# Optimization experiments

Hardware: AMD Instinct MI355X
Metric: run time of the kernel (lower is better)

The kernel has to match this reference:

```python
import jax, jax.numpy as jnp
import numpy as np

D_MODEL = 1024
NHEAD = 16
DK = D_MODEL // NHEAD  # 64
B, S = 2, 2048


def setup_inputs() -> dict:
    key = jax.random.key(0)
    ks = jax.random.split(key, 8)
    Q = jax.random.normal(ks[0], (B, S, D_MODEL), dtype=jnp.float32)
    K = jax.random.normal(ks[1], (B, S, D_MODEL), dtype=jnp.float32)
    V = jax.random.normal(ks[2], (B, S, D_MODEL), dtype=jnp.float32)
    additive_mask = jax.random.normal(ks[3], (S, S), dtype=jnp.float32)
    key_padding_mask = jnp.zeros((B, S), dtype=jnp.int32)  # ignored by the module
    # Per-head projection weights, stacked over heads: [H, d_model, dk]
    scale = 1.0 / np.sqrt(D_MODEL)
    WQ = jax.random.normal(ks[4], (NHEAD, D_MODEL, DK), dtype=jnp.float32) * scale
    WK = jax.random.normal(ks[5], (NHEAD, D_MODEL, DK), dtype=jnp.float32) * scale
    WV = jax.random.normal(ks[6], (NHEAD, D_MODEL, DK), dtype=jnp.float32) * scale
    WO = jax.random.normal(ks[7], (D_MODEL, D_MODEL), dtype=jnp.float32) * scale
    return {"Q": Q, "K": K, "V": V, "additive_mask": additive_mask,
            "key_padding_mask": key_padding_mask,
            "WQ": WQ, "WK": WK, "WV": WV, "WO": WO}


def reference(Q, K, V, additive_mask, key_padding_mask, WQ, WK, WV, WO):
    # Per-head projections, batched over heads: [B, H, S, dk]
    q = jnp.einsum('bsd,hdk->bhsk', Q, WQ)
    k = jnp.einsum('bsd,hdk->bhsk', K, WK)
    v = jnp.einsum('bsd,hdk->bhsk', V, WV)
    # scores: [B, H, S, S]; mask broadcasts over batch and head
    scores = jnp.einsum('bhqk,bhsk->bhqs', q, k) / np.sqrt(DK)
    scores = scores + additive_mask[None, None, :, :]
    attn = jax.nn.softmax(scores, axis=-1)
    o = jnp.einsum('bhqs,bhsk->bhqk', attn, v)  # [B, H, S, dk]
    # concat heads in head order == transpose + reshape to [B, S, H*dk]
    o = o.transpose(0, 2, 1, 3).reshape(Q.shape[0], Q.shape[1], D_MODEL)
    return o @ WO
```

## Files before the change

kernel.cpp:

```cpp
#include <hip/hip_runtime.h>
#include <hip/hip_bf16.h>
#include <stdint.h>

#define D_MODEL 1024
#define NHEAD 16
#define DKH 64
#define BATCH 2
#define SEQ 2048
#define LOG2E 1.44269504088896f

typedef __bf16 bf16_t;
typedef __bf16 bf16x8 __attribute__((ext_vector_type(8)));
typedef float f32x4 __attribute__((ext_vector_type(4)));

__device__ __forceinline__ float fast_exp2(float x) {
#if __has_builtin(__builtin_amdgcn_exp2f)
  return __builtin_amdgcn_exp2f(x);
#else
  return exp2f(x);
#endif
}

__device__ __forceinline__ void gload_lds16(const bf16_t* g, bf16_t* l) {
  auto gp = (const __attribute__((address_space(1))) void*)(uintptr_t)g;
  auto lp = (__attribute__((address_space(3))) void*)(uintptr_t)l;
  __builtin_amdgcn_global_load_lds(gp, lp, 16, 0, 0);
}

__global__ void k_cvtw(const float* __restrict__ WQ, const float* __restrict__ WK,
                       const float* __restrict__ WV, const float* __restrict__ WO,
                       bf16_t* __restrict__ wt) {
  int j = blockIdx.x * 256 + threadIdx.x;
  if (j < 3072 * 1024) {
    int bn = j >> 17, kt = (j >> 12) & 31, u = (j >> 10) & 3;
    int row = (j >> 3) & 127, e = j & 7;
    int n = bn * 128 + row;
    int d = kt * 32 + u * 8 + e;
    int proj = n >> 10, h = (n >> 6) & 15, k = n & 63;
    const float* w = proj == 0 ? WQ : (proj == 1 ? WK : WV);
    float scale = proj == 0 ? (0.125f * LOG2E) : 1.0f;
    wt[j] = (bf16_t)(w[(h << 16) + (d << 6) + k] * scale);
  } else {
    int j2 = j - 3072 * 1024;
    int bn = j2 >> 17, kt = (j2 >> 12) & 31, u = (j2 >> 10) & 3;
    int row = (j2 >> 3) & 127, e = j2 & 7;
    int n = bn * 128 + row;
    int d = kt * 32 + u * 8 + e;
    wt[j] = (bf16_t)WO[(d << 10) + n];
  }
}

__global__ void k_maskg(const float* __restrict__ M, bf16_t* __restrict__ Mf) {
  int t = blockIdx.x * 256 + threadIdx.x;
  int c = t & 3, lane = (t >> 2) & 63;
  int kvt = (t >> 8) & 31, qt16 = t >> 13;
  int q = qt16 * 16 + (lane & 15);
  int kv = kvt * 64 + c * 16 + ((lane >> 4) << 2);
  float4 m4 = *reinterpret_cast<const float4*>(M + (size_t)q * SEQ + kv);
  bf16_t o[4];
  o[0] = (bf16_t)(m4.x * LOG2E); o[1] = (bf16_t)(m4.y * LOG2E);
  o[2] = (bf16_t)(m4.z * LOG2E); o[3] = (bf16_t)(m4.w * LOG2E);
  *reinterpret_cast<ushort4*>(Mf + (size_t)t * 4) = *reinterpret_cast<ushort4*>(o);
}

__device__ __forceinline__ int vperm(int u) {
  return ((u >> 5) << 5) | (((u >> 2) & 3) << 3) | (((u >> 4) & 1) << 2) | (u & 3);
}

__global__ __launch_bounds__(256)
void k_gemm_qkv(const float* __restrict__ Qs, const float* __restrict__ Ks32,
                const float* __restrict__ Vs32, const bf16_t* __restrict__ Bt,
                bf16_t* __restrict__ qh, bf16_t* __restrict__ Kf,
                bf16_t* __restrict__ Vf) {
  __shared__ __align__(16) bf16_t As[4 * 128 * 8];
  __shared__ __align__(16) bf16_t Bs[4 * 128 * 8];
  const int tid = threadIdx.x;
  const int lane = tid & 63, wave = tid >> 6;
  const int g = lane >> 4, lr = lane & 15;
  const int bid = blockIdx.x;
  const int xcd = bid & 7, jj = bid >> 3;
  const int bm = xcd * 4 + (jj & 3);
  const int bn = jj >> 2;
  const int pn = bn >> 3;
  const float* Ap32 = pn == 0 ? Qs : (pn == 1 ? Ks32 : Vs32);
  const bf16_t* btile = Bt + (size_t)bn * 32 * 4096;
  const int wm = (wave >> 1) << 6, wn = (wave & 1) << 6;
  const int arow = tid >> 1, au0 = (tid & 1) << 1, ako = (tid & 1) << 4;
  const float* aptr = Ap32 + (size_t)(bm * 128 + arow) * 1024 + ako;
  f32x4 acc[4][4] = {};

  float4 fA0 = *reinterpret_cast<const float4*>(aptr);
  float4 fA1 = *reinterpret_cast<const float4*>(aptr + 4);
  float4 fA2 = *reinterpret_cast<const float4*>(aptr + 8);
  float4 fA3 = *reinterpret_cast<const float4*>(aptr + 12);

  for (int kt = 0; kt < 1024; kt += 32) {
    const int ktt = kt >> 5;
#pragma unroll
    for (int cc = 0; cc < 2; cc++) {
      int c = tid + cc * 256;
      gload_lds16(btile + (size_t)ktt * 4096 + c * 8, Bs + c * 8);
    }
    {
      bf16x8 o0, o1;
      o0[0] = (bf16_t)fA0.x; o0[1] = (bf16_t)fA0.y; o0[2] = (bf16_t)fA0.z; o0[3] = (bf16_t)fA0.w;
      o0[4] = (bf16_t)fA1.x; o0[5] = (bf16_t)fA1.y; o0[6] = (bf16_t)fA1.z; o0[7] = (bf16_t)fA1.w;
      o1[0] = (bf16_t)fA2.x; o1[1] = (bf16_t)fA2.y; o1[2] = (bf16_t)fA2.z; o1[3] = (bf16_t)fA2.w;
      o1[4] = (bf16_t)fA3.x; o1[5] = (bf16_t)fA3.y; o1[6] = (bf16_t)fA3.z; o1[7] = (bf16_t)fA3.w;
      *reinterpret_cast<bf16x8*>(As + (au0 * 128 + arow) * 8) = o0;
      *reinterpret_cast<bf16x8*>(As + ((au0 + 1) * 128 + arow) * 8) = o1;
    }
    if (kt + 32 < 1024) {
      const float* np = aptr + kt + 32;
      fA0 = *reinterpret_cast<const float4*>(np);
      fA1 = *reinterpret_cast<const float4*>(np + 4);
      fA2 = *reinterpret_cast<const float4*>(np + 8);
      fA3 = *reinterpret_cast<const float4*>(np + 12);
    }
    __syncthreads();
    bf16x8 af[4], bfr[4];
#pragma unroll
    for (int t = 0; t < 4; t++)
      af[t] = *reinterpret_cast<const bf16x8*>(As + (g * 128 + wm + t * 16 + lr) * 8);
#pragma unroll
    for (int t = 0; t < 4; t++)
      bfr[t] = *reinterpret_cast<const bf16x8*>(Bs + (g * 128 + wn + t * 16 + lr) * 8);
    __builtin_amdgcn_s_setprio(1);
#pragma unroll
    for (int i = 0; i < 4; i++)
#pragma unroll
      for (int j = 0; j < 4; j++)
        acc[i][j] = __builtin_amdgcn_mfma_f32_16x16x32_bf16(af[i], bfr[j], acc[i][j], 0, 0, 0);
    __builtin_amdgcn_s_setprio(0);
    __syncthreads();
  }

#pragma unroll
  for (int i = 0; i < 4; i++)
#pragma unroll
    for (int j = 0; j < 4; j++)
#pragma unroll
      for (int e = 0; e < 4; e++) {
        int row = (bm << 7) + wm + i * 16 + g * 4 + e;
        int col = ((bn & 7) << 7) + wn + j * 16 + lr;
        float v = acc[i][j][e];
        int b = row >> 11, s = row & 2047, h = col >> 6, d = col & 63;
        size_t tilebase = ((size_t)(((b << 4) + h) * 32) + (s >> 6)) * 4096;
        if (pn == 0) {
          qh[((size_t)(((b << 4) + h) * SEQ + s) << 6) + d] = (bf16_t)v;
        } else if (pn == 1) {
          int r = s & 63, u = (d >> 3) ^ (r & 7), e2 = d & 7;
          Kf[tilebase + r * 64 + u * 8 + e2] = (bf16_t)v;
        } else {
          int c6 = vperm(s & 63);
          int u = (c6 >> 3) ^ (d & 7), e2 = c6 & 7;
          Vf[tilebase + d * 64 + u * 8 + e2] = (bf16_t)v;
        }
      }
}

__global__ __launch_bounds__(256)
void k_gemm_wo(const bf16_t* __restrict__ A, const bf16_t* __restrict__ Bt,
               float* __restrict__ C) {
  __shared__ __align__(16) bf16_t As[64 * 32];
  __shared__ __align__(16) bf16_t Bs[4 * 128 * 8];
  const int tid = threadIdx.x;
  const int lane = tid & 63, wave = tid >> 6;
  const int g = lane >> 4, lr = lane & 15;
  const int bid = blockIdx.x;
  const int xcd = bid & 7, jj = bid >> 3;
  const int bm = xcd * 8 + (jj & 7);
  const int bn = jj >> 3;
  const bf16_t* btile = Bt + (size_t)bn * 32 * 4096;
  const int wm = (wave >> 1) << 5, wn = (wave & 1) << 6;
  f32x4 acc[2][4] = {};

  for (int kt = 0; kt < 1024; kt += 32) {
    const int ktt = kt >> 5;
    {
      int row = tid >> 2, ko = (tid & 3) << 3;
      gload_lds16(A + (size_t)(bm * 64 + row) * 1024 + kt + ko, As + tid * 8);
    }
#pragma unroll
    for (int cc = 0; cc < 2; cc++) {
      int c = tid + cc * 256;
      gload_lds16(btile + (size_t)ktt * 4096 + c * 8, Bs + c * 8);
    }
    __syncthreads();
    bf16x8 af[2], bfr[4];
#pragma unroll
    for (int t = 0; t < 2; t++)
      af[t] = *reinterpret_cast<const bf16x8*>(As + (wm + t * 16 + lr) * 32 + g * 8);
#pragma unroll
    for (int t = 0; t < 4; t++)
      bfr[t] = *reinterpret_cast<const bf16x8*>(Bs + (g * 128 + wn + t * 16 + lr) * 8);
    __builtin_amdgcn_s_setprio(1);
#pragma unroll
    for (int i = 0; i < 2; i++)
#pragma unroll
      for (int j = 0; j < 4; j++)
        acc[i][j] = __builtin_amdgcn_mfma_f32_16x16x32_bf16(af[i], bfr[j], acc[i][j], 0, 0, 0);
    __builtin_amdgcn_s_setprio(0);
    __syncthreads();
  }
#pragma unroll
  for (int i = 0; i < 2; i++)
#pragma unroll
    for (int j = 0; j < 4; j++)
#pragma unroll
      for (int e = 0; e < 4; e++) {
        int row = (bm << 6) + wm + i * 16 + g * 4 + e;
        int col = (bn << 7) + wn + j * 16 + lr;
        C[(size_t)row * D_MODEL + col] = acc[i][j][e];
      }
}

__global__ __launch_bounds__(512)
void k_attn4(const bf16_t* __restrict__ Qh, const bf16_t* __restrict__ Kf,
             const bf16_t* __restrict__ Vf, const bf16_t* __restrict__ Mf,
             bf16_t* __restrict__ O) {
  __shared__ __align__(16) bf16_t Ks[2][64 * 64];
  __shared__ __align__(16) bf16_t Vs[2][64 * 64];
  const int bid = blockIdx.x;
  const int xcd = bid & 7, loc = bid >> 3;
  const int bh = xcd * 4 + (loc >> 4);
  const int qtile = loc & 15;
  const int b = bh >> 4, h = bh & 15;
  const int tid = threadIdx.x, wave = tid >> 6, lane = tid & 63;
  const int g = lane >> 4, lr = lane & 15;
  const int qbase = qtile * 128 + wave * 16;
  const bf16_t* qp = Qh + (size_t)bh * SEQ * DKH;
  const bf16_t* kfp = Kf + (size_t)bh * 32 * 4096;
  const bf16_t* vfp = Vf + (size_t)bh * 32 * 4096;
  const int qt16 = qtile * 8 + wave;
  const bf16_t* mp = Mf + ((size_t)qt16 * 32 * 64 + lane) * 16;

  bf16x8 aq[2];
#pragma unroll
  for (int ks = 0; ks < 2; ks++)
    aq[ks] = *reinterpret_cast<const bf16x8*>(
        qp + (size_t)(qbase + lr) * DKH + ks * 32 + g * 8);

  f32x4 oacc[4] = {};
  f32x4 lacc = {};
  const bf16_t onev = (bf16_t)1.0f;
  const bf16x8 ones = {onev, onev, onev, onev, onev, onev, onev, onev};

  auto stage = [&](int buf, int kt) {
    gload_lds16(kfp + (size_t)kt * 4096 + tid * 8, &Ks[buf][tid * 8]);
    gload_lds16(vfp + (size_t)kt * 4096 + tid * 8, &Vs[buf][tid * 8]);
  };

  stage(0, 0);
  bf16x8 mva = *reinterpret_cast<const bf16x8*>(mp);
  bf16x8 mvb = *reinterpret_cast<const bf16x8*>(mp + 8);
  __syncthreads();

  for (int it = 0; it < SEQ / 64; ++it) {
    const int cur = it & 1;
    if (it + 1 < SEQ / 64) stage(cur ^ 1, it + 1);
    bf16x8 mna = mva, mnb = mvb;
    if (it + 1 < SEQ / 64) {
      const bf16_t* mn = mp + (size_t)(it + 1) * 1024;
      mna = *reinterpret_cast<const bf16x8*>(mn);
      mnb = *reinterpret_cast<const bf16x8*>(mn + 8);
    }

    const bf16_t* kb = Ks[cur];
    const bf16_t* vb = Vs[cur];

    f32x4 p[4];
#pragma unroll
    for (int c = 0; c < 4; c++) {
      int r = c * 16 + lr;
      bf16x8 bk0 = *reinterpret_cast<const bf16x8*>(kb + r * 64 + ((g ^ (lr & 7)) << 3));
      bf16x8 bk1 = *reinterpret_cast<const bf16x8*>(kb + r * 64 + (((4 + g) ^ (lr & 7)) << 3));
      __builtin_amdgcn_s_setprio(1);
      f32x4 a = {};
      a = __builtin_amdgcn_mfma_f32_16x16x32_bf16(bk0, aq[0], a, 0, 0, 0);
      a = __builtin_amdgcn_mfma_f32_16x16x32_bf16(bk1, aq[1], a, 0, 0, 0);
      __builtin_amdgcn_s_setprio(0);
      p[c] = a;
    }

    bf16x8 pa[2];
#pragma unroll
    for (int c = 0; c < 4; c++)
#pragma unroll
      for (int e = 0; e < 4; e++) {
        int idx = c * 4 + e;
        float mk = (float)(idx < 8 ? mva[idx] : mvb[idx - 8]);
        float x = p[c][e] + mk;
        float pe = fast_exp2(fminf(x, 60.f));
        pa[c >> 1][(c & 1) * 4 + e] = (bf16_t)pe;
      }

    lacc = __builtin_amdgcn_mfma_f32_16x16x32_bf16(pa[0], ones, lacc, 0, 0, 0);
    lacc = __builtin_amdgcn_mfma_f32_16x16x32_bf16(pa[1], ones, lacc, 0, 0, 0);

#pragma unroll
    for (int c2 = 0; c2 < 4; c2++) {
      int r = c2 * 16 + lr;
      bf16x8 bv0 = *reinterpret_cast<const bf16x8*>(vb + r * 64 + ((g ^ (lr & 7)) << 3));
      bf16x8 bv1 = *reinterpret_cast<const bf16x8*>(vb + r * 64 + (((4 + g) ^ (lr & 7)) << 3));
      __builtin_amdgcn_s_setprio(1);
      oacc[c2] = __builtin_amdgcn_mfma_f32_16x16x32_bf16(pa[0], bv0, oacc[c2], 0, 0, 0);
      oacc[c2] = __builtin_amdgcn_mfma_f32_16x16x32_bf16(pa[1], bv1, oacc[c2], 0, 0, 0);
      __builtin_amdgcn_s_setprio(0);
    }
    __syncthreads();
    mva = mna; mvb = mnb;
  }

  float inv[4];
#pragma unroll
  for (int e = 0; e < 4; e++) inv[e] = 1.0f / lacc[e];
#pragma unroll
  for (int c2 = 0; c2 < 4; c2++)
#pragma unroll
    for (int e = 0; e < 4; e++) {
      float v = oacc[c2][e] * inv[e];
      int row = qbase + g * 4 + e;
      int col = (h << 6) + c2 * 16 + lr;
      O[(size_t)(b * SEQ + row) * D_MODEL + col] = (bf16_t)v;
    }
}

extern "C" void kernel_launch(void* const* d_in, const int* in_sizes, int n_in,
                              void* d_out, int out_size, void* d_ws, size_t ws_size,
                              hipStream_t stream) {
  const float* Q  = (const float*)d_in[0];
  const float* K  = (const float*)d_in[1];
  const float* V  = (const float*)d_in[2];
  const float* M  = (const float*)d_in[3];
  const float* WQ = (const float*)d_in[5];
  const float* WK = (const float*)d_in[6];
  const float* WV = (const float*)d_in[7];
  const float* WO = (const float*)d_in[8];

  char* ws = (char*)d_ws;
  const size_t MB = 1 << 20;
  bf16_t* Mf    = (bf16_t*)(ws + 24 * MB);
  bf16_t* WqkvT = (bf16_t*)(ws + 32 * MB);
  bf16_t* WoT   = (bf16_t*)(ws + 38 * MB);
  bf16_t* qh    = (bf16_t*)(ws + 40 * MB);
  bf16_t* Kf    = (bf16_t*)(ws + 48 * MB);
  bf16_t* Vf    = (bf16_t*)(ws + 56 * MB);
  bf16_t* Ob    = (bf16_t*)(ws + 64 * MB);

  k_maskg<<<4096, 256, 0, stream>>>(M, Mf);
  k_cvtw<<<16384, 256, 0, stream>>>(WQ, WK, WV, WO, WqkvT);

  k_gemm_qkv<<<768, 256, 0, stream>>>(Q, K, V, WqkvT, qh, Kf, Vf);

  k_attn4<<<512, 512, 0, stream>>>(qh, Kf, Vf, Mf, Ob);

  k_gemm_wo<<<512, 256, 0, stream>>>(Ob, WoT, (float*)d_out);
}
```

Before: 135.7 us.

## Double-buffer LDS tiles in QKV and output projection GEMMs

Both projection GEMM kernels switch from single-buffered LDS to ping-pong buffers, so the next K-tile is loaded (and the fp32 A tile converted) into the alternate buffer while MFMAs consume the current one. The QKV kernel also keeps two register stages of fp32 A data to prefetch two tiles ahead, and its loop is fully unrolled. This aims to hide global/LDS load latency behind compute and drop one barrier per iteration, at the cost of doubled LDS use and higher register pressure, which may lower occupancy.

Result: slower. 138.5 us (+2.0%).

```diff
diff --git a/kernel.cpp b/kernel.cpp
--- a/kernel.cpp
+++ b/kernel.cpp
@@ -72,8 +72,8 @@
                 const float* __restrict__ Vs32, const bf16_t* __restrict__ Bt,
                 bf16_t* __restrict__ qh, bf16_t* __restrict__ Kf,
                 bf16_t* __restrict__ Vf) {
-  __shared__ __align__(16) bf16_t As[4 * 128 * 8];
-  __shared__ __align__(16) bf16_t Bs[4 * 128 * 8];
+  __shared__ __align__(16) bf16_t As[2][4 * 128 * 8];
+  __shared__ __align__(16) bf16_t Bs[2][4 * 128 * 8];
   const int tid = threadIdx.x;
   const int lane = tid & 63, wave = tid >> 6;
   const int g = lane >> 4, lr = lane & 15;
@@ -89,42 +89,68 @@
   const float* aptr = Ap32 + (size_t)(bm * 128 + arow) * 1024 + ako;
   f32x4 acc[4][4] = {};
 
-  float4 fA0 = *reinterpret_cast<const float4*>(aptr);
-  float4 fA1 = *reinterpret_cast<const float4*>(aptr + 4);
-  float4 fA2 = *reinterpret_cast<const float4*>(aptr + 8);
-  float4 fA3 = *reinterpret_cast<const float4*>(aptr + 12);
-
-  for (int kt = 0; kt < 1024; kt += 32) {
-    const int ktt = kt >> 5;
-#pragma unroll
-    for (int cc = 0; cc < 2; cc++) {
-      int c = tid + cc * 256;
-      gload_lds16(btile + (size_t)ktt * 4096 + c * 8, Bs + c * 8);
-    }
-    {
+  float4 sA[4], sB[4];
+#pragma unroll
+  for (int i = 0; i < 4; i++) sA[i] = *reinterpret_cast<const float4*>(aptr + i * 4);
+  {
+    bf16x8 o0, o1;
+    o0[0] = (bf16_t)sA[0].x; o0[1] = (bf16_t)sA[0].y; o0[2] = (bf16_t)sA[0].z; o0[3] = (bf16_t)sA[0].w;
+    o0[4] = (bf16_t)sA[1].x; o0[5] = (bf16_t)sA[1].y; o0[6] = (bf16_t)sA[1].z; o0[7] = (bf16_t)sA[1].w;
+    o1[0] = (bf16_t)sA[2].x; o1[1] = (bf16_t)sA[2].y; o1[2] = (bf16_t)sA[2].z; o1[3] = (bf16_t)sA[2].w;
+    o1[4] = (bf16_t)sA[3].x; o1[5] = (bf16_t)sA[3].y; o1[6] = (bf16_t)sA[3].z; o1[7] = (bf16_t)sA[3].w;
+    *reinterpret_cast<bf16x8*>(&As[0][(au0 * 128 + arow) * 8]) = o0;
+    *reinterpret_cast<bf16x8*>(&As[0][((au0 + 1) * 128 + arow) * 8]) = o1;
+  }
+#pragma unroll
+  for (int cc = 0; cc < 2; cc++) {
+    int c = tid + cc * 256;
+    gload_lds16(btile + c * 8, &Bs[0][c * 8]);
+  }
+#pragma unroll
+  for (int i = 0; i < 4; i++) sB[i] = *reinterpret_cast<const float4*>(aptr + 32 + i * 4);
+  __syncthreads();
+
+#pragma unroll
+  for (int t = 0; t < 32; ++t) {
+    const int c = t & 1;
+    if (t + 1 < 32) {
+#pragma unroll
+      for (int cc = 0; cc < 2; cc++) {
+        int ch = tid + cc * 256;
+        gload_lds16(btile + (size_t)(t + 1) * 4096 + ch * 8, &Bs[c ^ 1][ch * 8]);
+      }
       bf16x8 o0, o1;
-      o0[0] = (bf16_t)fA0.x; o0[1] = (bf16_t)fA0.y; o0[2] = (bf16_t)fA0.z; o0[3] = (bf16_t)fA0.w;
-      o0[4] = (bf16_t)fA1.x; o0[5] = (bf16_t)fA1.y; o0[6] = (bf16_t)fA1.z; o0[7] = (bf16_t)fA1.w;
-      o1[0] = (bf16_t)fA2.x; o1[1] = (bf16_t)fA2.y; o1[2] = (bf16_t)fA2.z; o1[3] = (bf16_t)fA2.w;
-      o1[4] = (bf16_t)fA3.x; o1[5] = (bf16_t)fA3.y; o1[6] = (bf16_t)fA3.z; o1[7] = (bf16_t)fA3.w;
-      *reinterpret_cast<bf16x8*>(As + (au0 * 128 + arow) * 8) = o0;
-      *reinterpret_cast<bf16x8*>(As + ((au0 + 1) * 128 + arow) * 8) = o1;
-    }
-    if (kt + 32 < 1024) {
-      const float* np = aptr + kt + 32;
-      fA0 = *reinterpret_cast<const float4*>(np);
-      fA1 = *reinterpret_cast<const float4*>(np + 4);
-      fA2 = *reinterpret_cast<const float4*>(np + 8);
-      fA3 = *reinterpret_cast<const float4*>(np + 12);
-    }
-    __syncthreads();
+      if ((t & 1) == 0) {
+        o0[0] = (bf16_t)sB[0].x; o0[1] = (bf16_t)sB[0].y; o0[2] = (bf16_t)sB[0].z; o0[3] = (bf16_t)sB[0].w;
+        o0[4] = (bf16_t)sB[1].x; o0[5] = (bf16_t)sB[1].y; o0[6] = (bf16_t)sB[1].z; o0[7] = (bf16_t)sB[1].w;
+        o1[0] = (bf16_t)sB[2].x; o1[1] = (bf16_t)sB[2].y; o1[2] = (bf16_t)sB[2].z; o1[3] = (bf16_t)sB[2].w;
+        o1[4] = (bf16_t)sB[3].x; o1[5] = (bf16_t)sB[3].y; o1[6] = (bf16_t)sB[3].z; o1[7] = (bf16_t)sB[3].w;
+      } else {
+        o0[0] = (bf16_t)sA[0].x; o0[1] = (bf16_t)sA[0].y; o0[2] = (bf16_t)sA[0].z; o0[3] = (bf16_t)sA[0].w;
+        o0[4] = (bf16_t)sA[1].x; o0[5] = (bf16_t)sA[1].y; o0[6] = (bf16_t)sA[1].z; o0[7] = (bf16_t)sA[1].w;
+        o1[0] = (bf16_t)sA[2].x; o1[1] = (bf16_t)sA[2].y; o1[2] = (bf16_t)sA[2].z; o1[3] = (bf16_t)sA[2].w;
+        o1[4] = (bf16_t)sA[3].x; o1[5] = (bf16_t)sA[3].y; o1[6] = (bf16_t)sA[3].z; o1[7] = (bf16_t)sA[3].w;
+      }
+      *reinterpret_cast<bf16x8*>(&As[c ^ 1][(au0 * 128 + arow) * 8]) = o0;
+      *reinterpret_cast<bf16x8*>(&As[c ^ 1][((au0 + 1) * 128 + arow) * 8]) = o1;
+    }
+    if (t + 2 < 32) {
+      const float* np = aptr + (size_t)(t + 2) * 32;
+      if ((t & 1) == 0) {
+#pragma unroll
+        for (int i = 0; i < 4; i++) sA[i] = *reinterpret_cast<const float4*>(np + i * 4);
+      } else {
+#pragma unroll
+        for (int i = 0; i < 4; i++) sB[i] = *reinterpret_cast<const float4*>(np + i * 4);
+      }
+    }
     bf16x8 af[4], bfr[4];
 #pragma unroll
-    for (int t = 0; t < 4; t++)
-      af[t] = *reinterpret_cast<const bf16x8*>(As + (g * 128 + wm + t * 16 + lr) * 8);
-#pragma unroll
-    for (int t = 0; t < 4; t++)
-      bfr[t] = *reinterpret_cast<const bf16x8*>(Bs + (g * 128 + wn + t * 16 + lr) * 8);
+    for (int q = 0; q < 4; q++)
+      af[q] = *reinterpret_cast<const bf16x8*>(&As[c][(g * 128 + wm + q * 16 + lr) * 8]);
+#pragma unroll
+    for (int q = 0; q < 4; q++)
+      bfr[q] = *reinterpret_cast<const bf16x8*>(&Bs[c][(g * 128 + wn + q * 16 + lr) * 8]);
     __builtin_amdgcn_s_setprio(1);
 #pragma unroll
     for (int i = 0; i < 4; i++)
@@ -162,8 +188,8 @@
 __global__ __launch_bounds__(256)
 void k_gemm_wo(const bf16_t* __restrict__ A, const bf16_t* __restrict__ Bt,
                float* __restrict__ C) {
-  __shared__ __align__(16) bf16_t As[64 * 32];
-  __shared__ __align__(16) bf16_t Bs[4 * 128 * 8];
+  __shared__ __align__(16) bf16_t As[2][64 * 32];
+  __shared__ __align__(16) bf16_t Bs[2][4 * 128 * 8];
   const int tid = threadIdx.x;
   const int lane = tid & 63, wave = tid >> 6;
   const int g = lane >> 4, lr = lane & 15;
@@ -175,25 +201,29 @@
   const int wm = (wave >> 1) << 5, wn = (wave & 1) << 6;
   f32x4 acc[2][4] = {};
 
-  for (int kt = 0; kt < 1024; kt += 32) {
-    const int ktt = kt >> 5;
-    {
-      int row = tid >> 2, ko = (tid & 3) << 3;
-      gload_lds16(A + (size_t)(bm * 64 + row) * 1024 + kt + ko, As + tid * 8);
-    }
+  auto stage = [&](int buf, int t) {
+    int row = tid >> 2, ko = (tid & 3) << 3;
+    gload_lds16(A + (size_t)(bm * 64 + row) * 1024 + t * 32 + ko, &As[buf][tid * 8]);
 #pragma unroll
     for (int cc = 0; cc < 2; cc++) {
       int c = tid + cc * 256;
-      gload_lds16(btile + (size_t)ktt * 4096 + c * 8, Bs + c * 8);
-    }
-    __syncthreads();
+      gload_lds16(btile + (size_t)t * 4096 + c * 8, &Bs[buf][c * 8]);
+    }
+  };
+
+  stage(0, 0);
+  __syncthreads();
+
+  for (int t = 0; t < 32; ++t) {
+    const int c = t & 1;
+    if (t + 1 < 32) stage(c ^ 1, t + 1);
     bf16x8 af[2], bfr[4];
 #pragma unroll
-    for (int t = 0; t < 2; t++)
-      af[t] = *reinterpret_cast<const bf16x8*>(As + (wm + t * 16 + lr) * 32 + g * 8);
-#pragma unroll
-    for (int t = 0; t < 4; t++)
-      bfr[t] = *reinterpret_cast<const bf16x8*>(Bs + (g * 128 + wn + t * 16 + lr) * 8);
+    for (int q = 0; q < 2; q++)
+      af[q] = *reinterpret_cast<const bf16x8*>(&As[c][(wm + q * 16 + lr) * 32 + g * 8]);
+#pragma unroll
+    for (int q = 0; q < 4; q++)
+      bfr[q] = *reinterpret_cast<const bf16x8*>(&Bs[c][(g * 128 + wn + q * 16 + lr) * 8]);
     __builtin_amdgcn_s_setprio(1);
 #pragma unroll
     for (int i = 0; i < 2; i++)
```
